# Kernel tuning notes

Hardware: AMD Instinct MI355X
Metric: run time of the kernel (lower is better)

## Reference

```python
import jax, jax.numpy as jnp
import numpy as np
import math

B = 1024
FV = 4096
E = 256
Z = E + 1
EPS = 1e-3
INNER_NSTEP = 8
INNER_LR = 0.5
NS = 16


def setup_inputs() -> dict:
    key = jax.random.key(0)
    ks = jax.random.split(key, 6)
    img = jax.random.uniform(ks[0], (B, FV), dtype=jnp.float32)
    lab = jax.random.randint(ks[1], (B,), 0, 10, dtype=jnp.int64)
    w_dec_w = jax.random.normal(ks[2], (FV, E), dtype=jnp.float32) / np.sqrt(E)
    w_dec_b = jnp.zeros((FV,), dtype=jnp.float32)
    whz_w = jax.random.normal(ks[3], (E, Z), dtype=jnp.float32) / np.sqrt(Z)
    whz_b = jnp.zeros((E,), dtype=jnp.float32)
    b_loc_prior = jax.random.normal(ks[4], (Z,), dtype=jnp.float32) * 0.1
    b_scale_out = jnp.zeros((), dtype=jnp.float32)
    return {"img": img, "lab": lab, "w_dec_w": w_dec_w, "w_dec_b": w_dec_b,
            "whz_w": whz_w, "whz_b": whz_b, "b_loc_prior": b_loc_prior,
            "b_scale_out": b_scale_out}


def reference(img, lab, w_dec_w, w_dec_b, whz_w, whz_b, b_loc_prior, b_scale_out):
    del lab  # unused by loss_joint_lp
    img_flat = img.reshape((img.shape[0], -1))  # [B, FV]
    Bn = img_flat.shape[0]
    node_h = jnp.full((Bn, E), EPS, dtype=img.dtype)
    node_z = jnp.full((Bn, Z), EPS, dtype=img.dtype)
    out_prec = jnp.exp(2.0 * b_scale_out)
    log_prior_sig = jax.nn.log_sigmoid(b_loc_prior)  # [Z]

    def step(carry, k):
        node_h, node_z = carry
        k1, k2 = jax.random.split(k)
        node_e = node_h @ w_dec_w.T + w_dec_b                     # [B, FV]
        dh1 = ((img_flat - node_e) * out_prec) @ w_dec_w          # [B, E]
        h_post_log = node_z @ whz_w.T + whz_b                     # [B, E]
        dh2 = jax.nn.log_sigmoid(h_post_log)
        dz1 = (node_h * jax.nn.sigmoid(-h_post_log)) @ whz_w + log_prior_sig  # [B, Z]
        h_next = jax.nn.sigmoid(dh1 + dh2)
        z_next = jax.nn.sigmoid(dz1)
        sel_h = jax.random.uniform(k1, node_h.shape) < INNER_LR
        sel_z = jax.random.uniform(k2, node_z.shape) < INNER_LR
        node_h = jnp.where(sel_h, 0.5 * (node_h + h_next), node_h)
        node_z = jnp.where(sel_z, 0.5 * (node_z + z_next), node_z)
        node_h = jax.lax.stop_gradient(node_h)  # mirrors .detach()
        node_z = jax.lax.stop_gradient(node_z)
        return (node_h, node_z), None

    loop_keys = jax.random.split(jax.random.key(42), INNER_NSTEP)
    (node_h, node_z), _ = jax.lax.scan(step, (node_h, node_z), loop_keys)

    # Importance-weighted bound with NS Bernoulli samples
    sk = jax.random.split(jax.random.key(7), 2)
    z_noise = (jax.random.uniform(sk[0], (NS, Bn, Z)) < node_z).astype(img.dtype)
    h_post_log = z_noise @ whz_w.T + whz_b                        # [NS, B, E]
    h_noise = (jax.random.uniform(sk[1], (NS, Bn, E)) < jax.nn.sigmoid(h_post_log)).astype(img.dtype)
    loc = h_noise @ w_dec_w.T + w_dec_b                           # [NS, B, FV]

    # Normal(loc, exp(b_scale_out)).log_prob(img_flat)
    inv_scale = jnp.exp(-b_scale_out)
    lp_external = (-0.5 * ((img_flat - loc) * inv_scale) ** 2
                   - b_scale_out - 0.5 * math.log(2.0 * math.pi))  # [NS, B, FV]

    # Bernoulli(logits=b_loc_prior).log_prob - Bernoulli(probs=node_z).log_prob
    lp_prior = z_noise * b_loc_prior - jax.nn.softplus(b_loc_prior)
    lp_post = z_noise * jnp.log(node_z) + (1.0 - z_noise) * jnp.log1p(-node_z)
    lp_internal = lp_prior - lp_post                               # [NS, B, Z]

    joint = lp_internal.sum(-1) + lp_external.sum(-1)              # [NS, B]
    lse = jax.nn.logsumexp(joint, axis=0) - math.log(NS)           # [B]
    return -lse.mean(0)
```

## Files before the change

kernel.cpp:

```cpp
#include <hip/hip_runtime.h>
#include <stdint.h>

#define B_    1024
#define FV_   4096
#define E_    256
#define Z_    257
#define NS_   16
#define NSB_  16384
#define EPS_  1e-3f

typedef __attribute__((ext_vector_type(8))) short short8v;
typedef __attribute__((ext_vector_type(4))) float f32x4;
#define MFMA16(a,b,c) __builtin_amdgcn_mfma_f32_16x16x32_bf16(a,b,c,0,0,0)

__host__ __device__ __forceinline__ uint32_t rotl32(uint32_t v, int r){
  return (v << r) | (v >> (32 - r));
}
__host__ __device__ __forceinline__ void tf2x32(uint32_t k0, uint32_t k1,
    uint32_t x0, uint32_t x1, uint32_t* o0, uint32_t* o1){
  uint32_t ks2 = k0 ^ k1 ^ 0x1BD11BDAu;
  x0 += k0; x1 += k1;
#define TFR(r) { x0 += x1; x1 = rotl32(x1, (r)); x1 ^= x0; }
  TFR(13) TFR(15) TFR(26) TFR(6)
  x0 += k1;  x1 += ks2 + 1u;
  TFR(17) TFR(29) TFR(16) TFR(24)
  x0 += ks2; x1 += k0 + 2u;
  TFR(13) TFR(15) TFR(26) TFR(6)
  x0 += k0;  x1 += k1 + 3u;
  TFR(17) TFR(29) TFR(16) TFR(24)
  x0 += k1;  x1 += ks2 + 4u;
  TFR(13) TFR(15) TFR(26) TFR(6)
  x0 += ks2; x1 += k0 + 5u;
#undef TFR
  *o0 = x0; *o1 = x1;
}
__device__ __forceinline__ uint64_t tf64(uint32_t k0, uint32_t k1, uint32_t c){
  uint32_t a, b; tf2x32(k0, k1, 0u, c, &a, &b);
  return ((uint64_t)b << 32) | (uint64_t)a;
}
__device__ __forceinline__ float u01(uint32_t bits){
  return __uint_as_float((bits >> 9) | 0x3f800000u) - 1.0f;
}
__device__ __forceinline__ float logsigf(float x){
  return fminf(x, 0.f) - __logf(1.f + __expf(-fabsf(x)));
}
__device__ __forceinline__ float sigf(float x){ return 1.f / (1.f + __expf(-x)); }
__device__ __forceinline__ unsigned short f2bf(float f){
  uint32_t b = __float_as_uint(f);
  return (unsigned short)((b + 0x7fffu + ((b >> 16) & 1u)) >> 16);
}
__device__ __forceinline__ float bf2f(unsigned short u){
  return __uint_as_float(((uint32_t)u) << 16);
}

__global__ void k_prepw(const float* __restrict__ whz,
                        unsigned short* __restrict__ whzPh,
                        unsigned short* __restrict__ whzTPh){
  int r = blockIdx.x, t = threadIdx.x;
  if (r < 256){
    for (int z = t; z < 288; z += 256)
      whzPh[(size_t)r * 288 + z] = (z < Z_) ? f2bf(whz[(size_t)r * Z_ + z]) : (unsigned short)0;
  }
  whzTPh[(size_t)r * 256 + t] = (r < Z_) ? f2bf(whz[(size_t)t * Z_ + r]) : (unsigned short)0;
}

__global__ __launch_bounds__(256) void k_prepimg(const float* __restrict__ img,
    const float* __restrict__ wb, unsigned short* __restrict__ imgb,
    float* __restrict__ r2){
  int b = blockIdx.x, t = threadIdx.x;
  float s = 0.f;
#pragma unroll
  for (int i = 0; i < 4; i++){
    int col = t * 4 + i * 1024;
    float4 v = *(const float4*)&img[(size_t)b * FV_ + col];
    float4 wv = *(const float4*)&wb[col];
    float d0 = v.x - wv.x, d1 = v.y - wv.y, d2 = v.z - wv.z, d3 = v.w - wv.w;
    s = fmaf(d0, d0, fmaf(d1, d1, fmaf(d2, d2, fmaf(d3, d3, s))));
    ushort4 o; o.x = f2bf(d0); o.y = f2bf(d1); o.z = f2bf(d2); o.w = f2bf(d3);
    *(ushort4*)&imgb[(size_t)b * FV_ + col] = o;
  }
  __shared__ float red[256];
  red[t] = s; __syncthreads();
  for (int w = 128; w > 0; w >>= 1){ if (t < w) red[t] += red[t + w]; __syncthreads(); }
  if (!t) r2[b] = red[0];
}

__global__ void k_prepwt(const float* __restrict__ W, unsigned short* __restrict__ Wt){
  __shared__ float ld[32][33];
  int f0 = blockIdx.x * 32, e0 = blockIdx.y * 32;
  int t = threadIdx.x, tx = t & 31, ty = t >> 5;
#pragma unroll
  for (int sub = 0; sub < 4; sub++){
    int r = ty + 8 * sub;
    ld[r][tx] = W[(size_t)(f0 + r) * 256 + e0 + tx];
  }
  __syncthreads();
#pragma unroll
  for (int sub = 0; sub < 4; sub++){
    int r = ty + 8 * sub;
    Wt[(size_t)(e0 + r) * 4096 + f0 + tx] = f2bf(ld[tx][r]);
  }
}

__global__ __launch_bounds__(256) void k_ata_mfma(const unsigned short* __restrict__ Wt,
                                                  float* __restrict__ part){
  int t = threadIdx.x, lane = t & 63, w = t >> 6, l15 = lane & 15, l4 = lane >> 4;
  int m0 = blockIdx.x * 16;
  size_t kc = (size_t)blockIdx.y * 256;
  f32x4 acc[4];
#pragma unroll
  for (int q = 0; q < 4; q++) acc[q] = (f32x4){0.f, 0.f, 0.f, 0.f};
  for (int kt = 0; kt < 8; kt++){
    short8v a = *(const short8v*)&Wt[(size_t)(m0 + l15) * 4096 + kc + kt * 32 + l4 * 8];
#pragma unroll
    for (int q = 0; q < 4; q++){
      short8v b = *(const short8v*)&Wt[(size_t)(w * 64 + q * 16 + l15) * 4096 + kc + kt * 32 + l4 * 8];
      acc[q] = MFMA16(a, b, acc[q]);
    }
  }
  float* dst = part + (size_t)blockIdx.y * 65536;
#pragma unroll
  for (int q = 0; q < 4; q++)
#pragma unroll
    for (int j = 0; j < 4; j++)
      dst[(size_t)(m0 + l4 * 4 + j) * 256 + w * 64 + q * 16 + l15] = acc[q][j];
}

__global__ __launch_bounds__(256) void k_pp_mfma(const unsigned short* __restrict__ imgb,
                                                 const unsigned short* __restrict__ Wt,
                                                 float* __restrict__ part){
  int t = threadIdx.x, lane = t & 63, w = t >> 6, l15 = lane & 15, l4 = lane >> 4;
  int m0 = blockIdx.x * 32;
  size_t kc = (size_t)blockIdx.y * 512;
  f32x4 acc0[4], acc1[4];
#pragma unroll
  for (int q = 0; q < 4; q++){ acc0[q] = (f32x4){0.f,0.f,0.f,0.f}; acc1[q] = (f32x4){0.f,0.f,0.f,0.f}; }
  for (int kt = 0; kt < 16; kt++){
    short8v a0 = *(const short8v*)&imgb[(size_t)(m0 + l15) * 4096 + kc + kt * 32 + l4 * 8];
    short8v a1 = *(const short8v*)&imgb[(size_t)(m0 + 16 + l15) * 4096 + kc + kt * 32 + l4 * 8];
#pragma unroll
    for (int q = 0; q < 4; q++){
      short8v b = *(const short8v*)&Wt[(size_t)(w * 64 + q * 16 + l15) * 4096 + kc + kt * 32 + l4 * 8];
      acc0[q] = MFMA16(a0, b, acc0[q]);
      acc1[q] = MFMA16(a1, b, acc1[q]);
    }
  }
  float* dst = part + (size_t)blockIdx.y * (B_ * 256);
#pragma unroll
  for (int q = 0; q < 4; q++)
#pragma unroll
    for (int j = 0; j < 4; j++){
      dst[(size_t)(m0 + l4 * 4 + j) * 256 + w * 64 + q * 16 + l15] = acc0[q][j];
      dst[(size_t)(m0 + 16 + l4 * 4 + j) * 256 + w * 64 + q * 16 + l15] = acc1[q][j];
    }
}

template<int P, bool BF>
__global__ void k_reduceP(const float* __restrict__ src, float* __restrict__ dstF,
                          unsigned short* __restrict__ dstH, int n){
  int i = blockIdx.x * 256 + threadIdx.x;
  if (i >= n) return;
  float s = 0.f;
#pragma unroll
  for (int p = 0; p < P; p++) s += src[(size_t)p * n + i];
  if (BF) dstH[i] = f2bf(s); else dstF[i] = s;
}

__global__ __launch_bounds__(512, 1) void k_inner(
    const unsigned short* __restrict__ whzPh,
    const unsigned short* __restrict__ whzTPh,
    const unsigned short* __restrict__ Gh,
    const float* __restrict__ whzb,
    const float* __restrict__ blp,
    const float* __restrict__ Pp,
    const float* __restrict__ bso,
    float* __restrict__ nzOut, float* __restrict__ cA, float* __restrict__ rowB,
    uint32_t hk00, uint32_t hk01, uint32_t hk10, uint32_t hk11,
    uint32_t zk00, uint32_t zk01, uint32_t zk10, uint32_t zk11)
{
  __shared__ unsigned short zb[16][296];
  __shared__ unsigned short hbuf[2][16][296];
  __shared__ unsigned short sgb[16][296];
  __shared__ float zl[16][260];
  __shared__ float ppl[16][256];
  __shared__ float lsb[272];
  __shared__ float xbl[272];
  __shared__ float w256l[256];
  __shared__ uint64_t hbitL[272][2];
  __shared__ uint64_t zbitL[272][2];

  const int t = threadIdx.x;
  const int lane = t & 63;
  const int w = t >> 6;
  const int l15 = lane & 15;
  const int l4 = lane >> 4;
  const int blk = blockIdx.x;
  const int b0 = blk * 16;
  const int n0 = w * 32 + l15;
  const int n1 = n0 + 16;

  const unsigned short epsb = f2bf(EPS_);
  for (int i = t; i < 16 * 296; i += 512){
    int r = i / 296, c = i % 296;
    zb[r][c] = (c < Z_) ? epsb : (unsigned short)0;
    hbuf[0][r][c] = (c < 256) ? epsb : (unsigned short)0;
    hbuf[1][r][c] = 0;
    sgb[r][c] = 0;
  }
  for (int i = t; i < 16 * 260; i += 512){
    int r = i / 260, c = i % 260;
    zl[r][c] = (c < Z_) ? EPS_ : 0.f;
  }
  for (int i = t; i < 4096; i += 512)
    ppl[i >> 8][i & 255] = Pp[(size_t)(b0 + (i >> 8)) * 256 + (i & 255)];
  if (t < 272){
    float x = (t < Z_) ? blp[t] : 0.f;
    xbl[t] = x;
    lsb[t] = logsigf(x);
    hbitL[t][0] = tf64(hk00, hk01, (uint32_t)(blk * 272 + t));
    hbitL[t][1] = tf64(hk10, hk11, (uint32_t)(blk * 272 + t));
    zbitL[t][0] = tf64(zk00, zk01, (uint32_t)(blk * 272 + t));
    zbitL[t][1] = tf64(zk10, zk11, (uint32_t)(blk * 272 + t));
  }
  if (t < 256) w256l[t] = bf2f(whzTPh[(size_t)256 * 256 + t]);

  const unsigned short* wApt0 = &whzPh[(size_t)n0 * 288 + l4 * 8];
  const unsigned short* wApt1 = &whzPh[(size_t)n1 * 288 + l4 * 8];
  const unsigned short* wBpt0 = &Gh[(size_t)n0 * 256 + l4 * 8];
  const unsigned short* wBpt1 = &Gh[(size_t)n1 * 256 + l4 * 8];
  const unsigned short* wCpt0 = &whzTPh[(size_t)n0 * 256 + l4 * 8];
  const unsigned short* wCpt1 = &whzTPh[(size_t)n1 * 256 + l4 * 8];
  const float w256A0 = bf2f(whzPh[(size_t)n0 * 288 + 256]);
  const float w256A1 = bf2f(whzPh[(size_t)n1 * 288 + 256]);
  const float op = __expf(2.f * bso[0]);
  const float wbr0 = whzb[n0], wbr1 = whzb[n1];
  const float lsr0 = logsigf(blp[n0]), lsr1 = logsigf(blp[n1]);
  const float lsr2 = logsigf(blp[256]);
  float hreg0[4] = {EPS_, EPS_, EPS_, EPS_};
  float hreg1[4] = {EPS_, EPS_, EPS_, EPS_};
  __syncthreads();

  for (int s = 0; s < 8; s++){
    const int sg = s >> 2, sh = (s & 3) << 4;
    const int cur = s & 1, nx = cur ^ 1;

    f32x4 aA0 = {0.f, 0.f, 0.f, 0.f};
    {
      short8v wt[8];
#pragma unroll
      for (int kt = 0; kt < 8; kt++) wt[kt] = *(const short8v*)(wApt0 + kt * 32);
#pragma unroll
      for (int kt = 0; kt < 8; kt++)
        aA0 = MFMA16(*(const short8v*)&zb[l15][kt * 32 + l4 * 8], wt[kt], aA0);
    }
    f32x4 aA1 = {0.f, 0.f, 0.f, 0.f};
    {
      short8v wt[8];
#pragma unroll
      for (int kt = 0; kt < 8; kt++) wt[kt] = *(const short8v*)(wApt1 + kt * 32);
#pragma unroll
      for (int kt = 0; kt < 8; kt++)
        aA1 = MFMA16(*(const short8v*)&zb[l15][kt * 32 + l4 * 8], wt[kt], aA1);
    }
    float d2r0[4], d2r1[4];
#pragma unroll
    for (int j = 0; j < 4; j++){
      int m = l4 * 4 + j;
      float z256v = bf2f(zb[m][256]);
      float hpl0 = aA0[j] + wbr0 + z256v * w256A0;
      float hpl1 = aA1[j] + wbr1 + z256v * w256A1;
      d2r0[j] = logsigf(hpl0);
      d2r1[j] = logsigf(hpl1);
      sgb[m][n0] = f2bf(hreg0[j] * sigf(-hpl0));
      sgb[m][n1] = f2bf(hreg1[j] * sigf(-hpl1));
    }
    __syncthreads();

    f32x4 aB0 = {0.f, 0.f, 0.f, 0.f};
    {
      short8v wt[8];
#pragma unroll
      for (int kt = 0; kt < 8; kt++) wt[kt] = *(const short8v*)(wBpt0 + kt * 32);
#pragma unroll
      for (int kt = 0; kt < 8; kt++)
        aB0 = MFMA16(*(const short8v*)&hbuf[cur][l15][kt * 32 + l4 * 8], wt[kt], aB0);
    }
    f32x4 aB1 = {0.f, 0.f, 0.f, 0.f};
    {
      short8v wt[8];
#pragma unroll
      for (int kt = 0; kt < 8; kt++) wt[kt] = *(const short8v*)(wBpt1 + kt * 32);
#pragma unroll
      for (int kt = 0; kt < 8; kt++)
        aB1 = MFMA16(*(const short8v*)&hbuf[cur][l15][kt * 32 + l4 * 8], wt[kt], aB1);
    }
    f32x4 aC0 = {0.f, 0.f, 0.f, 0.f};
    {
      short8v wt[8];
#pragma unroll
      for (int kt = 0; kt < 8; kt++) wt[kt] = *(const short8v*)(wCpt0 + kt * 32);
#pragma unroll
      for (int kt = 0; kt < 8; kt++)
        aC0 = MFMA16(*(const short8v*)&sgb[l15][kt * 32 + l4 * 8], wt[kt], aC0);
    }
    f32x4 aC1 = {0.f, 0.f, 0.f, 0.f};
    {
      short8v wt[8];
#pragma unroll
      for (int kt = 0; kt < 8; kt++) wt[kt] = *(const short8v*)(wCpt1 + kt * 32);
#pragma unroll
      for (int kt = 0; kt < 8; kt++)
        aC1 = MFMA16(*(const short8v*)&sgb[l15][kt * 32 + l4 * 8], wt[kt], aC1);
    }
    float zdot = 0.f;
    if (w == 0){
      int r = lane & 15, kg = lane >> 4;
#pragma unroll
      for (int c = 0; c < 8; c++){
        short8v sv = *(const short8v*)&sgb[r][kg * 64 + c * 8];
#pragma unroll
        for (int i = 0; i < 8; i++)
          zdot = fmaf(bf2f((unsigned short)sv[i]), w256l[kg * 64 + c * 8 + i], zdot);
      }
      zdot += __shfl_xor(zdot, 16);
      zdot += __shfl_xor(zdot, 32);
    }

    {
      uint64_t hb0w = hbitL[n0][sg], hb1w = hbitL[n1][sg];
#pragma unroll
      for (int j = 0; j < 4; j++){
        int m = l4 * 4 + j;
        float hn0 = sigf(op * (ppl[m][n0] - aB0[j]) + d2r0[j]);
        float hn1 = sigf(op * (ppl[m][n1] - aB1[j]) + d2r1[j]);
        if ((hb0w >> (sh | m)) & 1ull) hreg0[j] = 0.5f * (hreg0[j] + hn0);
        if ((hb1w >> (sh | m)) & 1ull) hreg1[j] = 0.5f * (hreg1[j] + hn1);
        hbuf[nx][m][n0] = f2bf(hreg0[j]);
        hbuf[nx][m][n1] = f2bf(hreg1[j]);
      }
    }
    {
      uint64_t zb0w = zbitL[n0][sg], zb1w = zbitL[n1][sg];
#pragma unroll
      for (int j = 0; j < 4; j++){
        int m = l4 * 4 + j;
        float zx0 = sigf(aC0[j] + lsr0);
        float old0 = zl[m][n0];
        float nz0 = ((zb0w >> (sh | m)) & 1ull) ? 0.5f * (old0 + zx0) : old0;
        zl[m][n0] = nz0; zb[m][n0] = f2bf(nz0);
        float zx1 = sigf(aC1[j] + lsr1);
        float old1 = zl[m][n1];
        float nz1 = ((zb1w >> (sh | m)) & 1ull) ? 0.5f * (old1 + zx1) : old1;
        zl[m][n1] = nz1; zb[m][n1] = f2bf(nz1);
      }
    }
    if (w == 0 && lane < 16){
      int r = lane;
      uint64_t zw = zbitL[256][sg];
      float zx = sigf(zdot + lsr2);
      float old = zl[r][256];
      float nz = ((zw >> (sh | r)) & 1ull) ? 0.5f * (old + zx) : old;
      zl[r][256] = nz; zb[r][256] = f2bf(nz);
    }
    __syncthreads();
  }

  {
    int r = t >> 5, g = t & 31;
    float s = 0.f;
    for (int c = g; c < Z_; c += 32){
      float pz = zl[r][c];
      float lgp = __logf(pz);
      float lgq = log1pf(-pz);
      float x = xbl[c];
      nzOut[(size_t)(b0 + r) * Z_ + c] = pz;
      cA[(size_t)(b0 + r) * Z_ + c] = x - lgp + lgq;
      s += -(x - lsb[c]) - lgq;
    }
#pragma unroll
    for (int m = 16; m >= 1; m >>= 1) s += __shfl_xor(s, m);
    if (g == 0) rowB[b0 + r] = s;
  }
}

__global__ __launch_bounds__(128) void k_znoise(const float* __restrict__ nzF,
    const float* __restrict__ cA, const float* __restrict__ rowB,
    unsigned short* __restrict__ znb, float* __restrict__ lpint,
    uint32_t k0, uint32_t k1){
  int r = blockIdx.x, t = threadIdx.x;
  int b = r & (B_ - 1);
  float acc = 0.f;
  uint32_t o0, o1;
  tf2x32(k0, k1, 0u, (uint32_t)(r * 130 + t), &o0, &o1);
  int z0 = 2 * t, z1 = 2 * t + 1;
  {
    float pz = nzF[(size_t)b * Z_ + z0];
    int zv = u01(o0) < pz;
    znb[(size_t)r * 288 + z0] = zv ? (unsigned short)0x3F80 : (unsigned short)0;
    if (zv) acc += cA[(size_t)b * Z_ + z0];
  }
  {
    float pz = nzF[(size_t)b * Z_ + z1];
    int zv = u01(o1) < pz;
    znb[(size_t)r * 288 + z1] = zv ? (unsigned short)0x3F80 : (unsigned short)0;
    if (zv) acc += cA[(size_t)b * Z_ + z1];
  }
  if (t == 0){
    uint32_t p0, p1;
    tf2x32(k0, k1, 0u, (uint32_t)(r * 130 + 128), &p0, &p1);
    float pz = nzF[(size_t)b * Z_ + 256];
    int zv = u01(p0) < pz;
    znb[(size_t)r * 288 + 256] = zv ? (unsigned short)0x3F80 : (unsigned short)0;
    if (zv) acc += cA[(size_t)b * Z_ + 256];
  }
  if (t < 31) znb[(size_t)r * 288 + 257 + t] = 0;
  __shared__ float red[128];
  red[t] = acc; __syncthreads();
  for (int w = 64; w > 0; w >>= 1){ if (t < w) red[t] += red[t + w]; __syncthreads(); }
  if (!t) lpint[r] = rowB[b] + red[0];
}

__global__ __launch_bounds__(256) void k_gemm1(const unsigned short* __restrict__ znb,
    const unsigned short* __restrict__ whzPh, const float* __restrict__ whzb,
    unsigned short* __restrict__ hnb, uint32_t k0, uint32_t k1){
  int t = threadIdx.x, lane = t & 63, w = t >> 6, l15 = lane & 15, l4 = lane >> 4;
  int m0 = blockIdx.x * 32;
  short8v af0[9], af1[9];
#pragma unroll
  for (int kt = 0; kt < 9; kt++){
    af0[kt] = *(const short8v*)&znb[(size_t)(m0 + l15) * 288 + kt * 32 + l4 * 8];
    af1[kt] = *(const short8v*)&znb[(size_t)(m0 + 16 + l15) * 288 + kt * 32 + l4 * 8];
  }
#pragma unroll
  for (int q = 0; q < 4; q++){
    int n = w * 64 + q * 16 + l15;
    f32x4 acc0 = {0.f, 0.f, 0.f, 0.f}, acc1 = {0.f, 0.f, 0.f, 0.f};
#pragma unroll
    for (int kt = 0; kt < 9; kt++){
      short8v b = *(const short8v*)&whzPh[(size_t)n * 288 + kt * 32 + l4 * 8];
      acc0 = MFMA16(af0[kt], b, acc0);
      acc1 = MFMA16(af1[kt], b, acc1);
    }
    float wbv = whzb[n];
#pragma unroll
    for (int i = 0; i < 2; i++){
      int rowbase = m0 + i * 16 + l4 * 4;
      uint32_t c0 = (uint32_t)((rowbase >> 1) * 256 + n);
      uint32_t a0, b0, a1, b1;
      tf2x32(k0, k1, 0u, c0, &a0, &b0);
      tf2x32(k0, k1, 0u, c0 + 256, &a1, &b1);
      float u[4] = {u01(a0), u01(b0), u01(a1), u01(b1)};
      const f32x4& ac = i ? acc1 : acc0;
#pragma unroll
      for (int j = 0; j < 4; j++){
        float pr = sigf(ac[j] + wbv);
        hnb[(size_t)(rowbase + j) * 256 + n] = (u[j] < pr) ? (unsigned short)0x3F80 : (unsigned short)0;
      }
    }
  }
}

__global__ __launch_bounds__(256) void k_gemm2(const unsigned short* __restrict__ hnb,
    const unsigned short* __restrict__ Gh, const float* __restrict__ Pp,
    const float* __restrict__ r2, const float* __restrict__ lpint,
    const float* __restrict__ bso, float* __restrict__ joint){
  int t = threadIdx.x, lane = t & 63, w = t >> 6, l15 = lane & 15, l4 = lane >> 4;
  int m0 = blockIdx.x * 32;
  short8v af0[8], af1[8];
#pragma unroll
  for (int kt = 0; kt < 8; kt++){
    af0[kt] = *(const short8v*)&hnb[(size_t)(m0 + l15) * 256 + kt * 32 + l4 * 8];
    af1[kt] = *(const short8v*)&hnb[(size_t)(m0 + 16 + l15) * 256 + kt * 32 + l4 * 8];
  }
  float s1a[4] = {0.f,0.f,0.f,0.f}, s2a[4] = {0.f,0.f,0.f,0.f};
  float s1b[4] = {0.f,0.f,0.f,0.f}, s2b[4] = {0.f,0.f,0.f,0.f};
#pragma unroll
  for (int q = 0; q < 4; q++){
    int n = w * 64 + q * 16 + l15;
    f32x4 acc0 = {0.f, 0.f, 0.f, 0.f}, acc1 = {0.f, 0.f, 0.f, 0.f};
#pragma unroll
    for (int kt = 0; kt < 8; kt++){
      short8v b = *(const short8v*)&Gh[(size_t)n * 256 + kt * 32 + l4 * 8];
      acc0 = MFMA16(af0[kt], b, acc0);
      acc1 = MFMA16(af1[kt], b, acc1);
    }
#pragma unroll
    for (int j = 0; j < 4; j++){
      int gm0 = m0 + l4 * 4 + j, gm1 = gm0 + 16;
      float hv0 = bf2f(hnb[(size_t)gm0 * 256 + n]);
      float hv1 = bf2f(hnb[(size_t)gm1 * 256 + n]);
      float pp0 = Pp[(size_t)(gm0 & (B_ - 1)) * 256 + n];
      float pp1 = Pp[(size_t)(gm1 & (B_ - 1)) * 256 + n];
      s1a[j] = fmaf(hv0, acc0[j], s1a[j]);
      s2a[j] = fmaf(hv0, pp0, s2a[j]);
      s1b[j] = fmaf(hv1, acc1[j], s1b[j]);
      s2b[j] = fmaf(hv1, pp1, s2b[j]);
    }
  }
#pragma unroll
  for (int j = 0; j < 4; j++){
#pragma unroll
    for (int msk = 1; msk < 16; msk <<= 1){
      s1a[j] += __shfl_xor(s1a[j], msk);
      s2a[j] += __shfl_xor(s2a[j], msk);
      s1b[j] += __shfl_xor(s1b[j], msk);
      s2b[j] += __shfl_xor(s2b[j], msk);
    }
  }
  __shared__ float sred[4][32][2];
  if (l15 == 0){
#pragma unroll
    for (int j = 0; j < 4; j++){
      sred[w][l4 * 4 + j][0] = s1a[j];
      sred[w][l4 * 4 + j][1] = s2a[j];
      sred[w][16 + l4 * 4 + j][0] = s1b[j];
      sred[w][16 + l4 * 4 + j][1] = s2b[j];
    }
  }
  __syncthreads();
  if (t < 32){
    float S1 = 0.f, S2 = 0.f;
#pragma unroll
    for (int wv = 0; wv < 4; wv++){ S1 += sred[wv][t][0]; S2 += sred[wv][t][1]; }
    int gm = m0 + t;
    int b = gm & (B_ - 1);
    float bs = bso[0];
    float isc2 = __expf(-2.f * bs);
    float se = r2[b] - 2.f * S2 + S1;
    joint[gm] = lpint[gm] - 0.5f * isc2 * se - (float)FV_ * (bs + 0.91893853320467274f);
  }
}

__global__ __launch_bounds__(1024) void k_final(const float* __restrict__ joint, float* __restrict__ out){
  int b = threadIdx.x;
  float mx = -3.0e38f;
  for (int n = 0; n < NS_; n++) mx = fmaxf(mx, joint[(size_t)n * B_ + b]);
  float s = 0.f;
  for (int n = 0; n < NS_; n++) s += __expf(joint[(size_t)n * B_ + b] - mx);
  float lse = mx + __logf(s) - 2.772588722239781f;
  __shared__ float red[1024];
  red[b] = lse; __syncthreads();
  for (int w = 512; w > 0; w >>= 1){ if (b < w) red[b] += red[b + w]; __syncthreads(); }
  if (!b) out[0] = -red[0] / (float)B_;
}

extern "C" void kernel_launch(void* const* d_in, const int* in_sizes, int n_in,
                              void* d_out, int out_size, void* d_ws, size_t ws_size,
                              hipStream_t stream){
  const float* img  = (const float*)d_in[0];
  const float* W    = (const float*)d_in[2];
  const float* wb   = (const float*)d_in[3];
  const float* whz  = (const float*)d_in[4];
  const float* whzb = (const float*)d_in[5];
  const float* blp  = (const float*)d_in[6];
  const float* bso  = (const float*)d_in[7];
  float* out = (float*)d_out;
  float* ws = (float*)d_ws;
  (void)in_sizes; (void)n_in; (void)out_size; (void)ws_size;

  size_t off = 0;
  auto nxt = [&](size_t n){ size_t o = off; off += (n + 63) & ~(size_t)63; return o; };
  float* Pp    = ws + nxt((size_t)B_ * 256);
  float* r2    = ws + nxt(B_);
  float* lpint = ws + nxt(NSB_);
  float* joint = ws + nxt(NSB_);
  float* nzF   = ws + nxt((size_t)B_ * Z_);
  float* cA    = ws + nxt((size_t)B_ * Z_);
  float* rowB  = ws + nxt(B_);
  unsigned short* Gh     = (unsigned short*)(ws + nxt((size_t)256 * 256 / 2));
  unsigned short* whzPh  = (unsigned short*)(ws + nxt((size_t)256 * 288 / 2));
  unsigned short* whzTPh = (unsigned short*)(ws + nxt((size_t)272 * 256 / 2));
  unsigned short* Wt     = (unsigned short*)(ws + nxt((size_t)256 * 4096 / 2));
  unsigned short* imgb   = (unsigned short*)(ws + nxt((size_t)B_ * FV_ / 2));
  float* znRgn = ws + nxt((size_t)NSB_ * 288 / 2);
  float* hnRgn = ws + nxt((size_t)NSB_ * 256 / 2);

  unsigned short* znb = (unsigned short*)znRgn;
  unsigned short* hnb = (unsigned short*)hnRgn;
  float* ataPart = znRgn;
  float* ppPart  = hnRgn;

  uint32_t hk00, hk01, hk10, hk11, zk00, zk01, zk10, zk11;
  tf2x32(0u, 42u, 1u, 0u, &hk00, &hk01);
  tf2x32(0u, 42u, 1u, 1u, &hk10, &hk11);
  tf2x32(0u, 42u, 2u, 0u, &zk00, &zk01);
  tf2x32(0u, 42u, 2u, 1u, &zk10, &zk11);
  uint32_t sk00, sk01, sk10, sk11;
  tf2x32(0u, 7u, 0u, 0u, &sk00, &sk01);
  tf2x32(0u, 7u, 0u, 1u, &sk10, &sk11);

  k_prepimg<<<dim3(B_), 256, 0, stream>>>(img, wb, imgb, r2);
  k_prepwt<<<dim3(128, 8), 256, 0, stream>>>(W, Wt);
  k_prepw<<<dim3(272), 256, 0, stream>>>(whz, whzPh, whzTPh);
  k_ata_mfma<<<dim3(16, 16), 256, 0, stream>>>(Wt, ataPart);
  k_reduceP<16, true><<<dim3(256), 256, 0, stream>>>(ataPart, nullptr, Gh, 65536);
  k_pp_mfma<<<dim3(32, 8), 256, 0, stream>>>(imgb, Wt, ppPart);
  k_reduceP<8, false><<<dim3(1024), 256, 0, stream>>>(ppPart, Pp, nullptr, B_ * 256);

  k_inner<<<dim3(64), 512, 0, stream>>>(whzPh, whzTPh, Gh, whzb, blp, Pp, bso,
                                        nzF, cA, rowB,
                                        hk00, hk01, hk10, hk11, zk00, zk01, zk10, zk11);

  k_znoise<<<dim3(NSB_), 128, 0, stream>>>(nzF, cA, rowB, znb, lpint, sk00, sk01);
  k_gemm1<<<dim3(512), 256, 0, stream>>>(znb, whzPh, whzb, hnb, sk10, sk11);
  k_gemm2<<<dim3(512), 256, 0, stream>>>(hnb, Gh, Pp, r2, lpint, bso, joint);
  k_final<<<dim3(1), 1024, 0, stream>>>(joint, out);
}
```

Baseline: 150.6 us.

## Fuse h-update into first GEMM phase and compute z[256] dot via MFMA

The per-step inner loop is restructured. The A and G weight GEMMs are interleaved per column tile, and the h-state update now runs before the barrier instead of after the C GEMM, so each step has one fewer dependent phase. The scalar wave-0 dot product for the last z column is replaced by an MFMA over whzT rows 256..271. log-sigmoid and sigmoid now share a single exp. The price is higher register pressure from holding more weight fragments, and reads of whzT rows past 256 that rely on the buffer being padded.

```diff
diff --git a/kernel.cpp b/kernel.cpp
--- a/kernel.cpp
+++ b/kernel.cpp
@@ -185,7 +185,6 @@
   __shared__ float ppl[16][256];
   __shared__ float lsb[272];
   __shared__ float xbl[272];
-  __shared__ float w256l[256];
   __shared__ uint64_t hbitL[272][2];
   __shared__ uint64_t zbitL[272][2];
 
@@ -222,14 +221,7 @@
     zbitL[t][0] = tf64(zk00, zk01, (uint32_t)(blk * 272 + t));
     zbitL[t][1] = tf64(zk10, zk11, (uint32_t)(blk * 272 + t));
   }
-  if (t < 256) w256l[t] = bf2f(whzTPh[(size_t)256 * 256 + t]);
-
-  const unsigned short* wApt0 = &whzPh[(size_t)n0 * 288 + l4 * 8];
-  const unsigned short* wApt1 = &whzPh[(size_t)n1 * 288 + l4 * 8];
-  const unsigned short* wBpt0 = &Gh[(size_t)n0 * 256 + l4 * 8];
-  const unsigned short* wBpt1 = &Gh[(size_t)n1 * 256 + l4 * 8];
-  const unsigned short* wCpt0 = &whzTPh[(size_t)n0 * 256 + l4 * 8];
-  const unsigned short* wCpt1 = &whzTPh[(size_t)n1 * 256 + l4 * 8];
+
   const float w256A0 = bf2f(whzPh[(size_t)n0 * 288 + 256]);
   const float w256A1 = bf2f(whzPh[(size_t)n1 * 288 + 256]);
   const float op = __expf(2.f * bso[0]);
@@ -244,99 +236,97 @@
     const int sg = s >> 2, sh = (s & 3) << 4;
     const int cur = s & 1, nx = cur ^ 1;
 
-    f32x4 aA0 = {0.f, 0.f, 0.f, 0.f};
+    f32x4 aA0 = {0.f, 0.f, 0.f, 0.f}, aB0 = {0.f, 0.f, 0.f, 0.f};
     {
-      short8v wt[8];
-#pragma unroll
-      for (int kt = 0; kt < 8; kt++) wt[kt] = *(const short8v*)(wApt0 + kt * 32);
-#pragma unroll
-      for (int kt = 0; kt < 8; kt++)
-        aA0 = MFMA16(*(const short8v*)&zb[l15][kt * 32 + l4 * 8], wt[kt], aA0);
-    }
-    f32x4 aA1 = {0.f, 0.f, 0.f, 0.f};
+      short8v wa[8], wg[8];
+#pragma unroll
+      for (int kt = 0; kt < 8; kt++){
+        wa[kt] = *(const short8v*)&whzPh[(size_t)n0 * 288 + kt * 32 + l4 * 8];
+        wg[kt] = *(const short8v*)&Gh[(size_t)n0 * 256 + kt * 32 + l4 * 8];
+      }
+#pragma unroll
+      for (int kt = 0; kt < 8; kt++){
+        short8v za = *(const short8v*)&zb[l15][kt * 32 + l4 * 8];
+        short8v ha = *(const short8v*)&hbuf[cur][l15][kt * 32 + l4 * 8];
+        aA0 = MFMA16(za, wa[kt], aA0);
+        aB0 = MFMA16(ha, wg[kt], aB0);
+      }
+    }
+    short8v wa1[8], wg1[8];
+#pragma unroll
+    for (int kt = 0; kt < 8; kt++){
+      wa1[kt] = *(const short8v*)&whzPh[(size_t)n1 * 288 + kt * 32 + l4 * 8];
+      wg1[kt] = *(const short8v*)&Gh[(size_t)n1 * 256 + kt * 32 + l4 * 8];
+    }
     {
-      short8v wt[8];
-#pragma unroll
-      for (int kt = 0; kt < 8; kt++) wt[kt] = *(const short8v*)(wApt1 + kt * 32);
-#pragma unroll
-      for (int kt = 0; kt < 8; kt++)
-        aA1 = MFMA16(*(const short8v*)&zb[l15][kt * 32 + l4 * 8], wt[kt], aA1);
-    }
-    float d2r0[4], d2r1[4];
-#pragma unroll
-    for (int j = 0; j < 4; j++){
-      int m = l4 * 4 + j;
-      float z256v = bf2f(zb[m][256]);
-      float hpl0 = aA0[j] + wbr0 + z256v * w256A0;
-      float hpl1 = aA1[j] + wbr1 + z256v * w256A1;
-      d2r0[j] = logsigf(hpl0);
-      d2r1[j] = logsigf(hpl1);
-      sgb[m][n0] = f2bf(hreg0[j] * sigf(-hpl0));
-      sgb[m][n1] = f2bf(hreg1[j] * sigf(-hpl1));
-    }
-    __syncthreads();
-
-    f32x4 aB0 = {0.f, 0.f, 0.f, 0.f};
-    {
-      short8v wt[8];
-#pragma unroll
-      for (int kt = 0; kt < 8; kt++) wt[kt] = *(const short8v*)(wBpt0 + kt * 32);
-#pragma unroll
-      for (int kt = 0; kt < 8; kt++)
-        aB0 = MFMA16(*(const short8v*)&hbuf[cur][l15][kt * 32 + l4 * 8], wt[kt], aB0);
-    }
-    f32x4 aB1 = {0.f, 0.f, 0.f, 0.f};
-    {
-      short8v wt[8];
-#pragma unroll
-      for (int kt = 0; kt < 8; kt++) wt[kt] = *(const short8v*)(wBpt1 + kt * 32);
-#pragma unroll
-      for (int kt = 0; kt < 8; kt++)
-        aB1 = MFMA16(*(const short8v*)&hbuf[cur][l15][kt * 32 + l4 * 8], wt[kt], aB1);
-    }
-    f32x4 aC0 = {0.f, 0.f, 0.f, 0.f};
-    {
-      short8v wt[8];
-#pragma unroll
-      for (int kt = 0; kt < 8; kt++) wt[kt] = *(const short8v*)(wCpt0 + kt * 32);
-#pragma unroll
-      for (int kt = 0; kt < 8; kt++)
-        aC0 = MFMA16(*(const short8v*)&sgb[l15][kt * 32 + l4 * 8], wt[kt], aC0);
-    }
-    f32x4 aC1 = {0.f, 0.f, 0.f, 0.f};
-    {
-      short8v wt[8];
-#pragma unroll
-      for (int kt = 0; kt < 8; kt++) wt[kt] = *(const short8v*)(wCpt1 + kt * 32);
-#pragma unroll
-      for (int kt = 0; kt < 8; kt++)
-        aC1 = MFMA16(*(const short8v*)&sgb[l15][kt * 32 + l4 * 8], wt[kt], aC1);
-    }
-    float zdot = 0.f;
-    if (w == 0){
-      int r = lane & 15, kg = lane >> 4;
-#pragma unroll
-      for (int c = 0; c < 8; c++){
-        short8v sv = *(const short8v*)&sgb[r][kg * 64 + c * 8];
-#pragma unroll
-        for (int i = 0; i < 8; i++)
-          zdot = fmaf(bf2f((unsigned short)sv[i]), w256l[kg * 64 + c * 8 + i], zdot);
-      }
-      zdot += __shfl_xor(zdot, 16);
-      zdot += __shfl_xor(zdot, 32);
-    }
-
-    {
-      uint64_t hb0w = hbitL[n0][sg], hb1w = hbitL[n1][sg];
+      uint64_t hb = hbitL[n0][sg];
 #pragma unroll
       for (int j = 0; j < 4; j++){
         int m = l4 * 4 + j;
-        float hn0 = sigf(op * (ppl[m][n0] - aB0[j]) + d2r0[j]);
-        float hn1 = sigf(op * (ppl[m][n1] - aB1[j]) + d2r1[j]);
-        if ((hb0w >> (sh | m)) & 1ull) hreg0[j] = 0.5f * (hreg0[j] + hn0);
-        if ((hb1w >> (sh | m)) & 1ull) hreg1[j] = 0.5f * (hreg1[j] + hn1);
+        float z256v = bf2f(zb[m][256]);
+        float hpl = aA0[j] + wbr0 + z256v * w256A0;
+        float e = __expf(-fabsf(hpl));
+        float den = 1.f + e;
+        float d2 = fminf(hpl, 0.f) - __logf(den);
+        float sgv = (hpl >= 0.f ? e : 1.f) / den;
+        sgb[m][n0] = f2bf(hreg0[j] * sgv);
+        float hn = sigf(op * (ppl[m][n0] - aB0[j]) + d2);
+        if ((hb >> (sh | m)) & 1ull) hreg0[j] = 0.5f * (hreg0[j] + hn);
         hbuf[nx][m][n0] = f2bf(hreg0[j]);
+      }
+    }
+    f32x4 aA1 = {0.f, 0.f, 0.f, 0.f}, aB1 = {0.f, 0.f, 0.f, 0.f};
+#pragma unroll
+    for (int kt = 0; kt < 8; kt++){
+      short8v za = *(const short8v*)&zb[l15][kt * 32 + l4 * 8];
+      short8v ha = *(const short8v*)&hbuf[cur][l15][kt * 32 + l4 * 8];
+      aA1 = MFMA16(za, wa1[kt], aA1);
+      aB1 = MFMA16(ha, wg1[kt], aB1);
+    }
+    {
+      uint64_t hb = hbitL[n1][sg];
+#pragma unroll
+      for (int j = 0; j < 4; j++){
+        int m = l4 * 4 + j;
+        float z256v = bf2f(zb[m][256]);
+        float hpl = aA1[j] + wbr1 + z256v * w256A1;
+        float e = __expf(-fabsf(hpl));
+        float den = 1.f + e;
+        float d2 = fminf(hpl, 0.f) - __logf(den);
+        float sgv = (hpl >= 0.f ? e : 1.f) / den;
+        sgb[m][n1] = f2bf(hreg1[j] * sgv);
+        float hn = sigf(op * (ppl[m][n1] - aB1[j]) + d2);
+        if ((hb >> (sh | m)) & 1ull) hreg1[j] = 0.5f * (hreg1[j] + hn);
         hbuf[nx][m][n1] = f2bf(hreg1[j]);
+      }
+    }
+    __syncthreads();
+
+    f32x4 aC0 = {0.f, 0.f, 0.f, 0.f}, aC1 = {0.f, 0.f, 0.f, 0.f};
+    {
+      short8v wc0[8], wc1[8];
+#pragma unroll
+      for (int kt = 0; kt < 8; kt++){
+        wc0[kt] = *(const short8v*)&whzTPh[(size_t)n0 * 256 + kt * 32 + l4 * 8];
+        wc1[kt] = *(const short8v*)&whzTPh[(size_t)n1 * 256 + kt * 32 + l4 * 8];
+      }
+#pragma unroll
+      for (int kt = 0; kt < 8; kt++){
+        short8v sa = *(const short8v*)&sgb[l15][kt * 32 + l4 * 8];
+        aC0 = MFMA16(sa, wc0[kt], aC0);
+        aC1 = MFMA16(sa, wc1[kt], aC1);
+      }
+    }
+    f32x4 aC2 = {0.f, 0.f, 0.f, 0.f};
+    if (w == 0){
+      short8v wc2[8];
+#pragma unroll
+      for (int kt = 0; kt < 8; kt++)
+        wc2[kt] = *(const short8v*)&whzTPh[(size_t)(256 + l15) * 256 + kt * 32 + l4 * 8];
+#pragma unroll
+      for (int kt = 0; kt < 8; kt++){
+        short8v sa = *(const short8v*)&sgb[l15][kt * 32 + l4 * 8];
+        aC2 = MFMA16(sa, wc2[kt], aC2);
       }
     }
     {
@@ -354,13 +344,16 @@
         zl[m][n1] = nz1; zb[m][n1] = f2bf(nz1);
       }
     }
-    if (w == 0 && lane < 16){
-      int r = lane;
+    if (w == 0 && l15 == 0){
       uint64_t zw = zbitL[256][sg];
-      float zx = sigf(zdot + lsr2);
-      float old = zl[r][256];
-      float nz = ((zw >> (sh | r)) & 1ull) ? 0.5f * (old + zx) : old;
-      zl[r][256] = nz; zb[r][256] = f2bf(nz);
+#pragma unroll
+      for (int j = 0; j < 4; j++){
+        int m = l4 * 4 + j;
+        float zx = sigf(aC2[j] + lsr2);
+        float old = zl[m][256];
+        float nz = ((zw >> (sh | m)) & 1ull) ? 0.5f * (old + zx) : old;
+        zl[m][256] = nz; zb[m][256] = f2bf(nz);
+      }
     }
     __syncthreads();
   }
```

After: 165.4 us. 1.1x slower.
